# Optimization experiments

Measured on AMD Instinct MI355X. Metric: run time of the kernel, lower is better.

The kernel has to match this reference:

```python
import jax, jax.numpy as jnp
import numpy as np

R = 0.2          # stable-distribution hash bucket width
TABLE_SIZE = 2   # hash table size (buckets)
M = 5            # number of appended ALSH transform dims
EPS = 1e-12


def conv2d(x, W, b, pad):
    out = jax.lax.conv_general_dilated(
        x, W, window_strides=(1, 1), padding=[(pad, pad), (pad, pad)],
        dimension_numbers=('NCHW', 'OIHW', 'NCHW'))
    return out + b[None, :, None, None]


def maxpool2(x):
    return jax.lax.reduce_window(x, -jnp.inf, jax.lax.max,
                                 (1, 1, 2, 2), (1, 1, 2, 2), 'VALID')


def alsh_mask(x, W, a, c):
    """ALSH filter selection: hash P(kernels) and Q(query) with a stable
    distribution hash h(v)=floor((a.v+b)/r) mod table_size; active filters
    are those landing in the query's bucket. Returns [B, Cout] 0/1 mask.
    Multiplying conv output by this mask == gather active filters then
    zero_fill_missing back to full channel count."""
    Cout, Cin, kH, kW = W.shape
    Kf = W.reshape(Cout, -1)                       # [Cout, Cin*kH*kW]
    norms = jnp.linalg.norm(Kf, axis=1)
    Kn = Kf / (jnp.max(norms) + EPS)               # scale so all norms <= 1
    n = jnp.linalg.norm(Kn, axis=1, keepdims=True)
    # P transform: append norm^2, norm^4, ..., norm^(2^M)
    powers = jnp.concatenate([n ** (2 ** (i + 1)) for i in range(M)], axis=1)
    P = jnp.concatenate([Kn, powers], axis=1)      # [Cout, d+M]
    kh = jnp.mod(jnp.floor((P @ a + c[0]) / R), TABLE_SIZE)  # [Cout]
    # query vector: per-sample channel means broadcast over kernel support
    cm = x.mean(axis=(2, 3))                       # [B, Cin]
    q = jnp.repeat(cm, kH * kW, axis=1)            # [B, Cin*kH*kW] (cin,kh,kw order)
    qn = q / (jnp.linalg.norm(q, axis=1, keepdims=True) + EPS)
    # Q transform: append M halves
    Qv = jnp.concatenate([qn, jnp.full((q.shape[0], M), 0.5, q.dtype)], axis=1)
    qh = jnp.mod(jnp.floor((Qv @ a + c[0]) / R), TABLE_SIZE)  # [B]
    return (kh[None, :] == qh[:, None]).astype(x.dtype)       # [B, Cout]


def setup_inputs() -> dict:
    key = jax.random.key(0)
    ks = jax.random.split(key, 16)
    u = lambda k, s: jax.random.uniform(k, s, jnp.float32, 0.0, R)
    n = lambda k, s, sc=0.1: jax.random.normal(k, s, jnp.float32) * sc
    return {
        'x': jax.random.normal(ks[0], (4096, 3, 32, 32), jnp.float32),
        'W1': n(ks[1], (16, 3, 5, 5)), 'b1': n(ks[2], (16,)),
        'a1': jax.random.normal(ks[3], (80,), jnp.float32), 'c1': u(ks[4], (1,)),
        'W2': n(ks[5], (20, 16, 5, 5)), 'b2': n(ks[6], (20,)),
        'a2': jax.random.normal(ks[7], (405,), jnp.float32), 'c2': u(ks[8], (1,)),
        'W3': n(ks[9], (20, 20, 5, 5)), 'b3': n(ks[10], (20,)),
        'a3': jax.random.normal(ks[11], (505,), jnp.float32), 'c3': u(ks[12], (1,)),
        'Wo': n(ks[13], (10, 320)), 'bo': n(ks[14], (10,)),
    }


def reference(x, W1, b1, a1, c1, W2, b2, a2, c2, W3, b3, a3, c3, Wo, bo):
    m1 = alsh_mask(x, W1, a1, c1)
    h = jax.nn.relu(conv2d(x, W1, b1, 2)) * m1[:, :, None, None]
    h = maxpool2(h)                                # [B,16,16,16]
    m2 = alsh_mask(h, W2, a2, c2)
    h = jax.nn.relu(conv2d(h, W2, b2, 2)) * m2[:, :, None, None]
    h = maxpool2(h)                                # [B,20,8,8]
    m3 = alsh_mask(h, W3, a3, c3)
    h = jax.nn.relu(conv2d(h, W3, b3, 2)) * m3[:, :, None, None]
    # zero_fill_missing -> identity here: inactive channels already zero
    h = maxpool2(h)                                # [B,20,4,4]
    flat = h.reshape(h.shape[0], -1)               # [B,320]
    return flat @ Wo.T + bo
```

## Files before the change

kernel.cpp:

```cpp
#include <hip/hip_runtime.h>
#include <hip/hip_bf16.h>

#define EPSV 1e-12
#define RHASH 0.2

__device__ __forceinline__ int fmod2(double t) {
    return (int)(((long long)floor(t)) & 1LL);
}

__device__ __forceinline__ void load_row6(const float* base, float* r) {
    float2 a0 = *(const float2*)(base);
    float2 a1 = *(const float2*)(base + 2);
    float2 a2 = *(const float2*)(base + 4);
    r[0] = a0.x; r[1] = a0.y; r[2] = a1.x; r[3] = a1.y; r[4] = a2.x; r[5] = a2.y;
}

#define FMA8(c,kx,w) { float wg=(w); \
  acc[c][0]=fmaf(wg,ca[kx],acc[c][0]); acc[c][1]=fmaf(wg,ca[(kx)+1],acc[c][1]); \
  acc[c][2]=fmaf(wg,na[kx],acc[c][2]); acc[c][3]=fmaf(wg,na[(kx)+1],acc[c][3]); \
  acc[c][4]=fmaf(wg,cb[kx],acc[c][4]); acc[c][5]=fmaf(wg,cb[(kx)+1],acc[c][5]); \
  acc[c][6]=fmaf(wg,nb[kx],acc[c][6]); acc[c][7]=fmaf(wg,nb[(kx)+1],acc[c][7]); }

#define FMA4(c,kx,w) { float wg=(w); \
  acc[c][0]=fmaf(wg,cur[kx],acc[c][0]); acc[c][1]=fmaf(wg,cur[(kx)+1],acc[c][1]); \
  acc[c][2]=fmaf(wg,nxt[kx],acc[c][2]); acc[c][3]=fmaf(wg,nxt[(kx)+1],acc[c][3]); }

__device__ void layer_setup(const float* W, const float* a, double cval,
                            int Co, int Ci, int* kh, double* asum, double* qc,
                            double* s_norm, float* Wbuf, float* abuf)
{
    const int t = threadIdx.x;
    const int D = Ci * 25;
    for (int i = t; i < Co * D; i += 256) Wbuf[i] = W[i];
    for (int i = t; i < D + 5; i += 256) abuf[i] = a[i];
    __syncthreads();
    if (t < Co) {
        double s = 0;
        for (int j = 0; j < D; ++j) { double w = (double)Wbuf[t * D + j]; s += w * w; }
        s_norm[t] = sqrt(s);
    }
    __syncthreads();
    if (t == 0) {
        double mx = 0;
        for (int i = 0; i < Co; ++i) mx = fmax(mx, s_norm[i]);
        s_norm[23] = 1.0 / (mx + EPSV);
    }
    __syncthreads();
    double scale = s_norm[23];
    if (t < Co) {
        double dp = 0;
        for (int j = 0; j < D; ++j) dp += (double)Wbuf[t * D + j] * (double)abuf[j];
        dp *= scale;
        double n = s_norm[t] * scale;
        double p = n * n;
        for (int m = 0; m < 5; ++m) { dp += p * (double)abuf[D + m]; p *= p; }
        kh[t] = fmod2((dp + cval) / RHASH);
    }
    if (t >= 64 && t < 64 + Ci) {
        int c = t - 64;
        double s = 0;
        for (int j = 0; j < 25; ++j) s += (double)abuf[c * 25 + j];
        asum[c] = s;
    }
    if (t == 128) {
        double s = 0;
        for (int m = 0; m < 5; ++m) s += (double)abuf[D + m];
        *qc = 0.5 * s + cval;
    }
    __syncthreads();
}

__global__ __launch_bounds__(256) void setup_kernel(
    const float* W1, const float* a1, const float* c1,
    const float* W2, const float* a2, const float* c2,
    const float* W3, const float* a3, const float* c3,
    double* dmeta, int* imeta)
{
    __shared__ float Wbuf[10000];
    __shared__ float abuf[512];
    __shared__ double s_norm[24];
    layer_setup(W1, a1, (double)c1[0], 16, 3,  imeta + 0,  dmeta + 0,  dmeta + 39, s_norm, Wbuf, abuf);
    layer_setup(W2, a2, (double)c2[0], 20, 16, imeta + 16, dmeta + 3,  dmeta + 40, s_norm, Wbuf, abuf);
    layer_setup(W3, a3, (double)c3[0], 20, 20, imeta + 36, dmeta + 19, dmeta + 41, s_norm, Wbuf, abuf);
}

__global__ __launch_bounds__(256) void pack_kernel(const float* W1, const float* W2, const float* W3,
                                                   float* Wp1, float* Wp2, float* Wp3)
{
    int i = blockIdx.x * 256 + threadIdx.x;
    if (i < 1200) {
        int co = i & 15, r = i >> 4;
        int kx = r % 5, r2 = r / 5, ky = r2 % 5, ci = r2 / 5;
        Wp1[i] = W1[co * 75 + ci * 25 + ky * 5 + kx];
    } else if (i < 1200 + 8960) {
        int k = i - 1200;
        int j = k % 28, r = k / 28;
        int cog = r % 4, r2 = r / 4, ky = r2 % 5, ci = r2 / 5;
        Wp2[k] = (j < 25) ? W2[(cog * 5 + j / 5) * 400 + ci * 25 + ky * 5 + (j % 5)] : 0.f;
    } else if (i < 1200 + 8960 + 11200) {
        int k = i - 10160;
        int j = k % 28, r = k / 28;
        int cog = r % 4, r2 = r / 4, ky = r2 % 5, ci = r2 / 5;
        Wp3[k] = (j < 25) ? W3[(cog * 5 + j / 5) * 500 + ci * 25 + ky * 5 + (j % 5)] : 0.f;
    }
}

__global__ __launch_bounds__(256, 4) void conv1_kernel(
    const float* __restrict__ x, const float* __restrict__ Wp1,
    const float* __restrict__ b1, const int* __restrict__ kh1,
    const double* __restrict__ dmeta, float* __restrict__ h1,
    int* __restrict__ qh2)
{
    __shared__ float xs[3][36][36];
    __shared__ float Ws[1200];
    __shared__ double s_red[3];
    __shared__ double s_ch[16][2];

    const int b = blockIdx.x, t = threadIdx.x;
    const int w = t >> 6, ln = t & 63;

    for (int i = t; i < 3 * 36 * 36; i += 256) (&xs[0][0][0])[i] = 0.f;
    for (int i = t; i < 600; i += 256) ((float2*)Ws)[i] = ((const float2*)Wp1)[i];
    __syncthreads();
    const float2* xb2 = (const float2*)(x + (size_t)b * 3072);
    for (int i = t; i < 1536; i += 256) {
        int idx = i * 2, c = idx >> 10, rem = idx & 1023;
        *(float2*)&xs[c][(rem >> 5) + 2][(rem & 31) + 2] = xb2[i];
    }
    __syncthreads();

    if (w < 3) {
        double s = 0;
        for (int j = 0; j < 16; ++j) {
            int i = ln + 64 * j;
            s += (double)xs[w][(i >> 5) + 2][(i & 31) + 2];
        }
        #pragma unroll
        for (int off = 32; off; off >>= 1) s += __shfl_xor(s, off);
        if (ln == 0) s_red[w] = s;
    }
    __syncthreads();
    double dp = 0, nn = 0;
    #pragma unroll
    for (int c = 0; c < 3; ++c) {
        double cm = s_red[c] * (1.0 / 1024.0);
        dp += cm * dmeta[c]; nn += cm * cm;
    }
    const int qh = fmod2((dp / (5.0 * sqrt(nn) + EPSV) + dmeta[39]) / RHASH);

    const int cog = t >> 7, r7 = t & 127;
    const int py = r7 >> 3, pxp = r7 & 7;
    const int y0 = 2 * py, x0a = 2 * pxp, x0b = 2 * pxp + 16;

    float acc[8][8];
    #pragma unroll
    for (int c = 0; c < 8; ++c) {
        float bb = b1[cog * 8 + c];
        #pragma unroll
        for (int j = 0; j < 8; ++j) acc[c][j] = bb;
    }

    #pragma unroll
    for (int ci = 0; ci < 3; ++ci) {
        #pragma unroll
        for (int ky = 0; ky < 5; ++ky) {
            float ca[6], na[6], cb[6], nb[6];
            load_row6(&xs[ci][y0 + ky][x0a],     ca);
            load_row6(&xs[ci][y0 + ky + 1][x0a], na);
            load_row6(&xs[ci][y0 + ky][x0b],     cb);
            load_row6(&xs[ci][y0 + ky + 1][x0b], nb);
            const float4* wq = (const float4*)&Ws[((ci * 5 + ky) * 5) * 16 + cog * 8];
            #pragma unroll
            for (int kx = 0; kx < 5; ++kx) {
                float4 w0 = wq[kx * 4];
                float4 w1 = wq[kx * 4 + 1];
                FMA8(0, kx, w0.x) FMA8(1, kx, w0.y) FMA8(2, kx, w0.z) FMA8(3, kx, w0.w)
                FMA8(4, kx, w1.x) FMA8(5, kx, w1.y) FMA8(6, kx, w1.z) FMA8(7, kx, w1.w)
            }
        }
    }

    float* hb = h1 + (size_t)b * 4096 + py * 16 + pxp;
    double csum[8];
    #pragma unroll
    for (int c = 0; c < 8; ++c) {
        int co = cog * 8 + c;
        float mask = (kh1[co] == qh) ? 1.f : 0.f;
        float mA = fmaxf(fmaxf(acc[c][0], acc[c][1]), fmaxf(acc[c][2], acc[c][3]));
        float mB = fmaxf(fmaxf(acc[c][4], acc[c][5]), fmaxf(acc[c][6], acc[c][7]));
        float vA = fmaxf(mA, 0.f) * mask;
        float vB = fmaxf(mB, 0.f) * mask;
        hb[co * 256]     = vA;
        hb[co * 256 + 8] = vB;
        csum[c] = (double)vA + (double)vB;
    }
    #pragma unroll
    for (int c = 0; c < 8; ++c) {
        double s = csum[c];
        #pragma unroll
        for (int off = 32; off; off >>= 1) s += __shfl_xor(s, off);
        if (ln == 0) s_ch[cog * 8 + c][w & 1] = s;
    }
    __syncthreads();
    if (t == 0) {
        double dp2 = 0, nn2 = 0;
        #pragma unroll
        for (int c = 0; c < 16; ++c) {
            double cm = (s_ch[c][0] + s_ch[c][1]) * (1.0 / 256.0);
            dp2 += cm * dmeta[3 + c]; nn2 += cm * cm;
        }
        qh2[b] = fmod2((dp2 / (5.0 * sqrt(nn2) + EPSV) + dmeta[40]) / RHASH);
    }
}

__global__ __launch_bounds__(256, 4) void conv2_kernel(
    const float* __restrict__ h1, const float* __restrict__ Wp2,
    const float* __restrict__ b2, const int* __restrict__ kh2,
    const int* __restrict__ qh2, const double* __restrict__ dmeta,
    float* __restrict__ h2, int* __restrict__ qh3)
{
    __shared__ float xs[2][4][20][20];
    __shared__ float Ws[2240];
    __shared__ double s_ch[2][20];

    const int b0 = blockIdx.x * 2, t = threadIdx.x;
    const int cog = t >> 6, slot = t & 63;
    const int s = slot >> 5, py = (slot >> 2) & 7, pxp = slot & 3;
    const int y0 = 2 * py, x0a = 2 * pxp, x0b = 2 * pxp + 8;

    for (int i = t; i < 3200; i += 256) (&xs[0][0][0][0])[i] = 0.f;

    const int qh = qh2[b0 + s];
    float acc[5][8];
    #pragma unroll
    for (int c = 0; c < 5; ++c) {
        float bb = b2[cog * 5 + c];
        #pragma unroll
        for (int j = 0; j < 8; ++j) acc[c][j] = bb;
    }
    __syncthreads();

    for (int ch = 0; ch < 4; ++ch) {
        for (int i = t; i < 1120; i += 256)
            ((float2*)Ws)[i] = ((const float2*)(Wp2 + ch * 2240))[i];
        for (int i = t; i < 1024; i += 256) {
            int ss = i >> 9, r = i & 511, ci = r >> 7, rr = r & 127, p2 = rr * 2;
            *(float2*)&xs[ss][ci][(p2 >> 4) + 2][(p2 & 15) + 2] =
                ((const float2*)(h1 + (size_t)(b0 + ss) * 4096 + (ch * 4 + ci) * 256))[rr];
        }
        __syncthreads();

        #pragma unroll
        for (int ci = 0; ci < 4; ++ci) {
            float ca[6], na[6], cb[6], nb[6];
            load_row6(&xs[s][ci][y0][x0a], ca);
            load_row6(&xs[s][ci][y0 + 1][x0a], na);
            load_row6(&xs[s][ci][y0][x0b], cb);
            load_row6(&xs[s][ci][y0 + 1][x0b], nb);
            #pragma unroll
            for (int ky = 0; ky < 5; ++ky) {
                const float* wrow = &Ws[((ci * 5 + ky) * 4 + cog) * 28];
                const float4* wq = (const float4*)wrow;
                float4 q;
                q = wq[0]; FMA8(0, 0, q.x) FMA8(0, 1, q.y) FMA8(0, 2, q.z) FMA8(0, 3, q.w)
                q = wq[1]; FMA8(0, 4, q.x) FMA8(1, 0, q.y) FMA8(1, 1, q.z) FMA8(1, 2, q.w)
                q = wq[2]; FMA8(1, 3, q.x) FMA8(1, 4, q.y) FMA8(2, 0, q.z) FMA8(2, 1, q.w)
                q = wq[3]; FMA8(2, 2, q.x) FMA8(2, 3, q.y) FMA8(2, 4, q.z) FMA8(3, 0, q.w)
                q = wq[4]; FMA8(3, 1, q.x) FMA8(3, 2, q.y) FMA8(3, 3, q.z) FMA8(3, 4, q.w)
                q = wq[5]; FMA8(4, 0, q.x) FMA8(4, 1, q.y) FMA8(4, 2, q.z) FMA8(4, 3, q.w)
                FMA8(4, 4, wrow[24])
                if (ky < 4) {
                    #pragma unroll
                    for (int j = 0; j < 6; ++j) { ca[j] = na[j]; cb[j] = nb[j]; }
                    load_row6(&xs[s][ci][y0 + ky + 2][x0a], na);
                    load_row6(&xs[s][ci][y0 + ky + 2][x0b], nb);
                }
            }
        }
        __syncthreads();
    }

    float* ob = h2 + (size_t)(b0 + s) * 1280 + py * 8 + pxp;
    double csum[5];
    #pragma unroll
    for (int c = 0; c < 5; ++c) {
        int co = cog * 5 + c;
        float mask = (kh2[co] == qh) ? 1.f : 0.f;
        float mA = fmaxf(fmaxf(acc[c][0], acc[c][1]), fmaxf(acc[c][2], acc[c][3]));
        float mB = fmaxf(fmaxf(acc[c][4], acc[c][5]), fmaxf(acc[c][6], acc[c][7]));
        float vA = fmaxf(mA, 0.f) * mask;
        float vB = fmaxf(mB, 0.f) * mask;
        ob[co * 64]     = vA;
        ob[co * 64 + 4] = vB;
        csum[c] = (double)vA + (double)vB;
    }
    #pragma unroll
    for (int c = 0; c < 5; ++c) {
        double sv = csum[c];
        #pragma unroll
        for (int off = 16; off; off >>= 1) sv += __shfl_xor(sv, off);
        if ((slot & 31) == 0) s_ch[s][cog * 5 + c] = sv;
    }
    __syncthreads();
    if (t < 2) {
        double dp2 = 0, nn2 = 0;
        #pragma unroll
        for (int c = 0; c < 20; ++c) {
            double cm = s_ch[t][c] * (1.0 / 64.0);
            dp2 += cm * dmeta[19 + c]; nn2 += cm * cm;
        }
        qh3[b0 + t] = fmod2((dp2 / (5.0 * sqrt(nn2) + EPSV) + dmeta[41]) / RHASH);
    }
}

__global__ __launch_bounds__(256, 4) void conv3_kernel(
    const float* __restrict__ h2, const float* __restrict__ Wp3,
    const float* __restrict__ b3, const int* __restrict__ kh3,
    const int* __restrict__ qh3,
    const float* __restrict__ Wo, const float* __restrict__ bo,
    float* __restrict__ out, int B)
{
    __shared__ float xs[4][5][12][12];
    __shared__ float Ws[2800];
    __shared__ float flat[4][320];

    const int b0 = blockIdx.x * 4, t = threadIdx.x;
    const int s = t >> 6, q0 = t & 63, cog = q0 >> 4, pos = q0 & 15;
    const int py = pos >> 2, px = pos & 3;
    const int y0 = 2 * py, x0 = 2 * px;
    const int b = b0 + s;

    for (int i = t; i < 4 * 5 * 144; i += 256) (&xs[0][0][0][0])[i] = 0.f;

    const int qh = (b < B) ? qh3[b] : 0;
    float acc[5][4];
    #pragma unroll
    for (int c = 0; c < 5; ++c) {
        float bb = b3[cog * 5 + c];
        acc[c][0] = bb; acc[c][1] = bb; acc[c][2] = bb; acc[c][3] = bb;
    }
    __syncthreads();

    for (int ch = 0; ch < 4; ++ch) {
        for (int i = t; i < 1400; i += 256)
            ((float2*)Ws)[i] = ((const float2*)(Wp3 + ch * 2800))[i];
        for (int i = t; i < 640; i += 256) {
            int ss = i / 160, r = i - ss * 160, ci = r >> 5, rr = r & 31, p2 = rr * 2;
            if (b0 + ss < B)
                *(float2*)&xs[ss][ci][(p2 >> 3) + 2][(p2 & 7) + 2] =
                    ((const float2*)(h2 + (size_t)(b0 + ss) * 1280 + (ch * 5 + ci) * 64))[rr];
        }
        __syncthreads();

        #pragma unroll
        for (int ci = 0; ci < 5; ++ci) {
            float cur[6], nxt[6];
            load_row6(&xs[s][ci][y0][x0], cur);
            load_row6(&xs[s][ci][y0 + 1][x0], nxt);
            #pragma unroll
            for (int ky = 0; ky < 5; ++ky) {
                const float* wrow = &Ws[((ci * 5 + ky) * 4 + cog) * 28];
                const float4* wq = (const float4*)wrow;
                float4 q;
                q = wq[0]; FMA4(0, 0, q.x) FMA4(0, 1, q.y) FMA4(0, 2, q.z) FMA4(0, 3, q.w)
                q = wq[1]; FMA4(0, 4, q.x) FMA4(1, 0, q.y) FMA4(1, 1, q.z) FMA4(1, 2, q.w)
                q = wq[2]; FMA4(1, 3, q.x) FMA4(1, 4, q.y) FMA4(2, 0, q.z) FMA4(2, 1, q.w)
                q = wq[3]; FMA4(2, 2, q.x) FMA4(2, 3, q.y) FMA4(2, 4, q.z) FMA4(3, 0, q.w)
                q = wq[4]; FMA4(3, 1, q.x) FMA4(3, 2, q.y) FMA4(3, 3, q.z) FMA4(3, 4, q.w)
                q = wq[5]; FMA4(4, 0, q.x) FMA4(4, 1, q.y) FMA4(4, 2, q.z) FMA4(4, 3, q.w)
                FMA4(4, 4, wrow[24])
                if (ky < 4) {
                    #pragma unroll
                    for (int j = 0; j < 6; ++j) cur[j] = nxt[j];
                    load_row6(&xs[s][ci][y0 + ky + 2][x0], nxt);
                }
            }
        }
        __syncthreads();
    }

    #pragma unroll
    for (int c = 0; c < 5; ++c) {
        int co = cog * 5 + c;
        float m = fmaxf(fmaxf(acc[c][0], acc[c][1]), fmaxf(acc[c][2], acc[c][3]));
        flat[s][co * 16 + pos] = fmaxf(m, 0.f) * ((kh3[co] == qh) ? 1.f : 0.f);
    }
    __syncthreads();

    if (t < 160) {
        const int g = t >> 2, qq = t & 3;
        const int ss = g / 10, o = g - ss * 10;
        float a = 0.f;
        const float* wr = Wo + o * 320;
        for (int k = qq; k < 320; k += 4) a = fmaf(flat[ss][k], wr[k], a);
        a += __shfl_xor(a, 1);
        a += __shfl_xor(a, 2);
        if (qq == 0 && b0 + ss < B) out[(size_t)(b0 + ss) * 10 + o] = a + bo[o];
    }
}

extern "C" void kernel_launch(void* const* d_in, const int* in_sizes, int n_in,
                              void* d_out, int out_size, void* d_ws, size_t ws_size,
                              hipStream_t stream)
{
    const float* x  = (const float*)d_in[0];
    const float* W1 = (const float*)d_in[1];
    const float* b1 = (const float*)d_in[2];
    const float* a1 = (const float*)d_in[3];
    const float* c1 = (const float*)d_in[4];
    const float* W2 = (const float*)d_in[5];
    const float* b2 = (const float*)d_in[6];
    const float* a2 = (const float*)d_in[7];
    const float* c2 = (const float*)d_in[8];
    const float* W3 = (const float*)d_in[9];
    const float* b3 = (const float*)d_in[10];
    const float* a3 = (const float*)d_in[11];
    const float* c3 = (const float*)d_in[12];
    const float* Wo = (const float*)d_in[13];
    const float* bo = (const float*)d_in[14];
    float* out = (float*)d_out;

    const int B = in_sizes[0] / 3072;

    float* h1  = (float*)d_ws;
    float* h2  = h1 + (size_t)B * 4096;
    float* Wp1 = h2 + (size_t)B * 1280;
    float* Wp2 = Wp1 + 1200;
    float* Wp3 = Wp2 + 8960;
    double* dmeta = (double*)(Wp3 + 11200);
    int* imeta = (int*)(dmeta + 42);
    int* qh2 = imeta + 56;
    int* qh3 = qh2 + B;

    setup_kernel<<<1, 256, 0, stream>>>(W1, a1, c1, W2, a2, c2, W3, a3, c3, dmeta, imeta);
    pack_kernel<<<84, 256, 0, stream>>>(W1, W2, W3, Wp1, Wp2, Wp3);
    conv1_kernel<<<B, 256, 0, stream>>>(x, Wp1, b1, imeta, dmeta, h1, qh2);
    conv2_kernel<<<B / 2, 256, 0, stream>>>(h1, Wp2, b2, imeta + 16, qh2, dmeta, h2, qh3);
    conv3_kernel<<<(B + 3) / 4, 256, 0, stream>>>(h2, Wp3, b3, imeta + 36, qh3, Wo, bo, out, B);
}
```

Measured before the change: 570.2 us.

## Restructure conv2 to one sample per block with 8-channel input chunks

Conv2 now processes one sample per block instead of two. Each thread computes one pooled output (4 conv positions) per channel instead of two, and input channels are staged in two chunks of 8 instead of four chunks of 4, which halves the barrier and reload rounds. Weights are loaded into registers per row and the input rows are reloaded per ky rather than rolled through registers. The min-blocks launch bound hint is dropped from all three conv kernels. This doubles the grid size and lowers per-thread register pressure, but reduces register reuse of input rows and doubles LDS use per block.

```diff
diff --git a/kernel.cpp b/kernel.cpp
--- a/kernel.cpp
+++ b/kernel.cpp
@@ -105,7 +105,7 @@
     }
 }
 
-__global__ __launch_bounds__(256, 4) void conv1_kernel(
+__global__ __launch_bounds__(256) void conv1_kernel(
     const float* __restrict__ x, const float* __restrict__ Wp1,
     const float* __restrict__ b1, const int* __restrict__ kh1,
     const double* __restrict__ dmeta, float* __restrict__ h1,
@@ -213,107 +213,104 @@
     }
 }
 
-__global__ __launch_bounds__(256, 4) void conv2_kernel(
+__global__ __launch_bounds__(256) void conv2_kernel(
     const float* __restrict__ h1, const float* __restrict__ Wp2,
     const float* __restrict__ b2, const int* __restrict__ kh2,
     const int* __restrict__ qh2, const double* __restrict__ dmeta,
     float* __restrict__ h2, int* __restrict__ qh3)
 {
-    __shared__ float xs[2][4][20][20];
-    __shared__ float Ws[2240];
-    __shared__ double s_ch[2][20];
-
-    const int b0 = blockIdx.x * 2, t = threadIdx.x;
-    const int cog = t >> 6, slot = t & 63;
-    const int s = slot >> 5, py = (slot >> 2) & 7, pxp = slot & 3;
-    const int y0 = 2 * py, x0a = 2 * pxp, x0b = 2 * pxp + 8;
-
-    for (int i = t; i < 3200; i += 256) (&xs[0][0][0][0])[i] = 0.f;
-
-    const int qh = qh2[b0 + s];
-    float acc[5][8];
+    __shared__ float xs[8][20][20];
+    __shared__ float Ws[4480];
+    __shared__ double s_ch[20];
+
+    const int b = blockIdx.x, t = threadIdx.x;
+    const int cog = t >> 6, pos = t & 63;
+    const int py = pos >> 3, px = pos & 7;
+    const int y0 = 2 * py, x0 = 2 * px;
+
+    for (int i = t; i < 3200; i += 256) (&xs[0][0][0])[i] = 0.f;
+
+    const int qh = qh2[b];
+    float acc[5][4];
     #pragma unroll
     for (int c = 0; c < 5; ++c) {
         float bb = b2[cog * 5 + c];
-        #pragma unroll
-        for (int j = 0; j < 8; ++j) acc[c][j] = bb;
-    }
-    __syncthreads();
-
-    for (int ch = 0; ch < 4; ++ch) {
-        for (int i = t; i < 1120; i += 256)
-            ((float2*)Ws)[i] = ((const float2*)(Wp2 + ch * 2240))[i];
+        acc[c][0] = bb; acc[c][1] = bb; acc[c][2] = bb; acc[c][3] = bb;
+    }
+    __syncthreads();
+
+    for (int ch = 0; ch < 2; ++ch) {
+        for (int i = t; i < 2240; i += 256)
+            ((float2*)Ws)[i] = ((const float2*)(Wp2 + ch * 4480))[i];
+        const float2* src = (const float2*)(h1 + (size_t)b * 4096 + ch * 2048);
         for (int i = t; i < 1024; i += 256) {
-            int ss = i >> 9, r = i & 511, ci = r >> 7, rr = r & 127, p2 = rr * 2;
-            *(float2*)&xs[ss][ci][(p2 >> 4) + 2][(p2 & 15) + 2] =
-                ((const float2*)(h1 + (size_t)(b0 + ss) * 4096 + (ch * 4 + ci) * 256))[rr];
+            int ci = i >> 7, r = i & 127, p2 = r * 2;
+            *(float2*)&xs[ci][(p2 >> 4) + 2][(p2 & 15) + 2] = src[i];
         }
         __syncthreads();
 
-        #pragma unroll
-        for (int ci = 0; ci < 4; ++ci) {
-            float ca[6], na[6], cb[6], nb[6];
-            load_row6(&xs[s][ci][y0][x0a], ca);
-            load_row6(&xs[s][ci][y0 + 1][x0a], na);
-            load_row6(&xs[s][ci][y0][x0b], cb);
-            load_row6(&xs[s][ci][y0 + 1][x0b], nb);
+        for (int ci = 0; ci < 8; ++ci) {
             #pragma unroll
             for (int ky = 0; ky < 5; ++ky) {
-                const float* wrow = &Ws[((ci * 5 + ky) * 4 + cog) * 28];
-                const float4* wq = (const float4*)wrow;
-                float4 q;
-                q = wq[0]; FMA8(0, 0, q.x) FMA8(0, 1, q.y) FMA8(0, 2, q.z) FMA8(0, 3, q.w)
-                q = wq[1]; FMA8(0, 4, q.x) FMA8(1, 0, q.y) FMA8(1, 1, q.z) FMA8(1, 2, q.w)
-                q = wq[2]; FMA8(1, 3, q.x) FMA8(1, 4, q.y) FMA8(2, 0, q.z) FMA8(2, 1, q.w)
-                q = wq[3]; FMA8(2, 2, q.x) FMA8(2, 3, q.y) FMA8(2, 4, q.z) FMA8(3, 0, q.w)
-                q = wq[4]; FMA8(3, 1, q.x) FMA8(3, 2, q.y) FMA8(3, 3, q.z) FMA8(3, 4, q.w)
-                q = wq[5]; FMA8(4, 0, q.x) FMA8(4, 1, q.y) FMA8(4, 2, q.z) FMA8(4, 3, q.w)
-                FMA8(4, 4, wrow[24])
-                if (ky < 4) {
+                float xr0[6], xr1[6];
+                load_row6(&xs[ci][y0 + ky][x0],     xr0);
+                load_row6(&xs[ci][y0 + ky + 1][x0], xr1);
+                float wv[28];
+                const float4* wp = (const float4*)&Ws[((ci * 5 + ky) * 4 + cog) * 28];
+                *(float4*)&wv[0]  = wp[0];
+                *(float4*)&wv[4]  = wp[1];
+                *(float4*)&wv[8]  = wp[2];
+                *(float4*)&wv[12] = wp[3];
+                *(float4*)&wv[16] = wp[4];
+                *(float4*)&wv[20] = wp[5];
+                *(float4*)&wv[24] = wp[6];
+                #pragma unroll
+                for (int c = 0; c < 5; ++c) {
                     #pragma unroll
-                    for (int j = 0; j < 6; ++j) { ca[j] = na[j]; cb[j] = nb[j]; }
-                    load_row6(&xs[s][ci][y0 + ky + 2][x0a], na);
-                    load_row6(&xs[s][ci][y0 + ky + 2][x0b], nb);
+                    for (int kx = 0; kx < 5; ++kx) {
+                        float wgt = wv[c * 5 + kx];
+                        acc[c][0] = fmaf(wgt, xr0[kx],     acc[c][0]);
+                        acc[c][1] = fmaf(wgt, xr0[kx + 1], acc[c][1]);
+                        acc[c][2] = fmaf(wgt, xr1[kx],     acc[c][2]);
+                        acc[c][3] = fmaf(wgt, xr1[kx + 1], acc[c][3]);
+                    }
                 }
             }
         }
         __syncthreads();
     }
 
-    float* ob = h2 + (size_t)(b0 + s) * 1280 + py * 8 + pxp;
+    float* ob = h2 + (size_t)b * 1280 + pos;
     double csum[5];
     #pragma unroll
     for (int c = 0; c < 5; ++c) {
         int co = cog * 5 + c;
         float mask = (kh2[co] == qh) ? 1.f : 0.f;
-        float mA = fmaxf(fmaxf(acc[c][0], acc[c][1]), fmaxf(acc[c][2], acc[c][3]));
-        float mB = fmaxf(fmaxf(acc[c][4], acc[c][5]), fmaxf(acc[c][6], acc[c][7]));
-        float vA = fmaxf(mA, 0.f) * mask;
-        float vB = fmaxf(mB, 0.f) * mask;
-        ob[co * 64]     = vA;
-        ob[co * 64 + 4] = vB;
-        csum[c] = (double)vA + (double)vB;
+        float m = fmaxf(fmaxf(acc[c][0], acc[c][1]), fmaxf(acc[c][2], acc[c][3]));
+        float v = fmaxf(m, 0.f) * mask;
+        ob[co * 64] = v;
+        csum[c] = (double)v;
     }
     #pragma unroll
     for (int c = 0; c < 5; ++c) {
         double sv = csum[c];
         #pragma unroll
-        for (int off = 16; off; off >>= 1) sv += __shfl_xor(sv, off);
-        if ((slot & 31) == 0) s_ch[s][cog * 5 + c] = sv;
-    }
-    __syncthreads();
-    if (t < 2) {
+        for (int off = 32; off; off >>= 1) sv += __shfl_xor(sv, off);
+        if (pos == 0) s_ch[cog * 5 + c] = sv;
+    }
+    __syncthreads();
+    if (t == 0) {
         double dp2 = 0, nn2 = 0;
         #pragma unroll
         for (int c = 0; c < 20; ++c) {
-            double cm = s_ch[t][c] * (1.0 / 64.0);
+            double cm = s_ch[c] * (1.0 / 64.0);
             dp2 += cm * dmeta[19 + c]; nn2 += cm * cm;
         }
-        qh3[b0 + t] = fmod2((dp2 / (5.0 * sqrt(nn2) + EPSV) + dmeta[41]) / RHASH);
-    }
-}
-
-__global__ __launch_bounds__(256, 4) void conv3_kernel(
+        qh3[b] = fmod2((dp2 / (5.0 * sqrt(nn2) + EPSV) + dmeta[41]) / RHASH);
+    }
+}
+
+__global__ __launch_bounds__(256) void conv3_kernel(
     const float* __restrict__ h2, const float* __restrict__ Wp3,
     const float* __restrict__ b3, const int* __restrict__ kh3,
     const int* __restrict__ qh3,
@@ -435,6 +432,6 @@
     setup_kernel<<<1, 256, 0, stream>>>(W1, a1, c1, W2, a2, c2, W3, a3, c3, dmeta, imeta);
     pack_kernel<<<84, 256, 0, stream>>>(W1, W2, W3, Wp1, Wp2, Wp3);
     conv1_kernel<<<B, 256, 0, stream>>>(x, Wp1, b1, imeta, dmeta, h1, qh2);
-    conv2_kernel<<<B / 2, 256, 0, stream>>>(h1, Wp2, b2, imeta + 16, qh2, dmeta, h2, qh3);
+    conv2_kernel<<<B, 256, 0, stream>>>(h1, Wp2, b2, imeta + 16, qh2, dmeta, h2, qh3);
     conv3_kernel<<<(B + 3) / 4, 256, 0, stream>>>(h2, Wp3, b3, imeta + 36, qh3, Wo, bo, out, B);
 }
```

Measured after the change: 522.7 us. 8.3% less time.
